# Kernel tuning notes

Hardware: AMD Instinct MI355X
Metric: run time of the kernel (lower is better)

The kernel has to match this reference:

```python
import jax, jax.numpy as jnp
import numpy as np

N_NODES = 20000   # N
N_EDGES = 320000  # E (avg degree 16)
T_STEPS = 16      # T
IN_FEATS = 1      # F
HG = 64           # hidden_g
HT = 128          # hidden_t
LN_EPS = 1e-5


def _layer_norm(x, g, b):
    mu = jnp.mean(x, axis=-1, keepdims=True)
    var = jnp.mean((x - mu) ** 2, axis=-1, keepdims=True)
    return (x - mu) * jax.lax.rsqrt(var + LN_EPS) * g + b


def setup_inputs() -> dict:
    key = jax.random.key(0)
    k = jax.random.split(key, 16)
    r = lambda i, shape, s: jax.random.normal(k[i], shape, jnp.float32) * s
    return dict(
        x_seq=jax.random.normal(k[0], (1, T_STEPS, N_NODES, IN_FEATS), jnp.float32),
        edge_index=jax.random.randint(k[1], (2, N_EDGES), 0, N_NODES, dtype=jnp.int32),
        # SAGEConv layer 0: lin_l (aggregated neighbors, has bias) + lin_r (root)
        W_l0=r(2, (IN_FEATS, HG), 0.5), W_r0=r(3, (IN_FEATS, HG), 0.5), b0=jnp.zeros((HG,), jnp.float32),
        ln0_g=jnp.ones((HG,), jnp.float32), ln0_b=jnp.zeros((HG,), jnp.float32),
        # SAGEConv layer 1
        W_l1=r(4, (HG, HG), 0.1), W_r1=r(5, (HG, HG), 0.1), b1=jnp.zeros((HG,), jnp.float32),
        ln1_g=jnp.ones((HG,), jnp.float32), ln1_b=jnp.zeros((HG,), jnp.float32),
        # GRU (torch layout: gates r,z,n stacked along first dim)
        gru_Wih=r(6, (3 * HT, HG), 0.05), gru_Whh=r(7, (3 * HT, HT), 0.05),
        gru_bih=jnp.zeros((3 * HT,), jnp.float32), gru_bhh=jnp.zeros((3 * HT,), jnp.float32),
        # head
        head_W=r(8, (HT, 1), 0.05), head_b=jnp.zeros((1,), jnp.float32),
    )


def reference(x_seq, edge_index, W_l0, W_r0, b0, ln0_g, ln0_b,
              W_l1, W_r1, b1, ln1_g, ln1_b,
              gru_Wih, gru_Whh, gru_bih, gru_bhh, head_W, head_b):
    src, dst = edge_index[0], edge_index[1]
    # in-degree for mean aggregation (clamped to 1, like PyG mean aggr on isolated nodes)
    deg = jnp.clip(jax.ops.segment_sum(jnp.ones((N_EDGES,), jnp.float32), dst,
                                       num_segments=N_NODES), 1.0)[:, None]

    def sage(x, Wl, Wr, b):
        # mean over incoming neighbors, then lin_l(aggr) + lin_r(root)
        agg = jax.ops.segment_sum(x[src], dst, num_segments=N_NODES) / deg
        return agg @ Wl + x @ Wr + b

    def stack(xt):  # xt: (N, F) -> (N, HG); dropout is identity in eval mode
        h = jax.nn.relu(_layer_norm(sage(xt, W_l0, W_r0, b0), ln0_g, ln0_b))
        h = jax.nn.relu(_layer_norm(sage(h, W_l1, W_r1, b1), ln1_g, ln1_b))
        return h

    X = x_seq[0]  # (T, N, F), B == 1
    # scan over timesteps (matches the per-t Python loop, bounds peak memory)
    _, H = jax.lax.scan(lambda c, xt: (c, stack(xt)), None, X)  # H: (T, N, HG)

    def gru_step(h, xt):  # torch GRU cell; batch = N nodes
        gi = xt @ gru_Wih.T + gru_bih
        gh = h @ gru_Whh.T + gru_bhh
        ir, iz, inn = jnp.split(gi, 3, axis=-1)
        hr, hz, hn = jnp.split(gh, 3, axis=-1)
        r = jax.nn.sigmoid(ir + hr)
        z = jax.nn.sigmoid(iz + hz)
        n = jnp.tanh(inn + r * hn)
        return (1.0 - z) * n + z * h, None

    h0 = jnp.zeros((N_NODES, HT), x_seq.dtype)
    hT, _ = jax.lax.scan(gru_step, h0, H)
    y = (hT @ head_W + head_b)[:, 0]  # (N,)
    return y
```

## Files before the change

### kernel.cpp

```cpp
#include <hip/hip_runtime.h>
#include <math.h>

#define NN 20000
#define NE 320000
#define TS 16
#define HG 64
#define HTT 128
#define NG 384
#define LN_EPS 1e-5f

typedef __attribute__((ext_vector_type(8))) _Float16 f16x8;
typedef __attribute__((ext_vector_type(4))) _Float16 f16x4;
typedef __attribute__((ext_vector_type(2))) _Float16 f16x2;
typedef __attribute__((ext_vector_type(4))) float f32x4;

__device__ __forceinline__ float wave_sum64(float v) {
  #pragma unroll
  for (int off = 32; off > 0; off >>= 1) v += __shfl_xor(v, off, 64);
  return v;
}
__device__ __forceinline__ float quad_sum16(float v) {
  #pragma unroll
  for (int off = 1; off < 16; off <<= 1) v += __shfl_xor(v, off, 64);
  return v;
}
__device__ __forceinline__ float fast_sigmoid(float x) {
  return __builtin_amdgcn_rcpf(1.f + __expf(-x));
}
__device__ __forceinline__ float fast_tanh(float x) {
  float e = __expf(-2.f * fabsf(x));
  float th = (1.f - e) * __builtin_amdgcn_rcpf(1.f + e);
  return copysignf(th, x);
}


__global__ __launch_bounds__(256) void k_setup(
    const float* __restrict__ x_seq, float* __restrict__ xT,
    const float* __restrict__ Wih, _Float16* __restrict__ WihF,
    const float* __restrict__ Whh, _Float16* __restrict__ WhhF,
    const float* __restrict__ Wl1, const float* __restrict__ Wr1,
    _Float16* __restrict__ Wchi, _Float16* __restrict__ Wclo,
    const float* __restrict__ Wl0, const float* __restrict__ Wr0,
    const float* __restrict__ b0, const float* __restrict__ g0,
    const float* __restrict__ be0, float* __restrict__ P,
    int* __restrict__ cnt) {
  int gid = blockIdx.x * 256 + threadIdx.x;
  int stride = gridDim.x * 256;
  for (int i = gid; i < NN * TS; i += stride) {
    int t = i / NN, n = i - t * NN;
    xT[n * 16 + t] = x_seq[i];
  }
  for (int i = gid; i < NG * HG; i += stride) WihF[i] = (_Float16)Wih[i];
  for (int i = gid; i < NG * HTT; i += stride) WhhF[i] = (_Float16)Whh[i];
  for (int i = gid; i < HG * 128; i += stride) {
    int n = i >> 7, k = i & 127;
    float x = (k < HG) ? Wl1[k * HG + n] : Wr1[(k - HG) * HG + n];
    _Float16 h = (_Float16)x;
    Wchi[i] = h;
    Wclo[i] = (_Float16)(x - (float)h);
  }
  for (int i = gid; i < NN; i += stride) cnt[i] = 0;
  if (blockIdx.x == 0 && threadIdx.x < 64) {
    int f = threadIdx.x;
    float u = Wl0[f], v = Wr0[f], c = b0[f], g = g0[f];
    float um = wave_sum64(u) * (1.f / 64.f);
    float vm = wave_sum64(v) * (1.f / 64.f);
    float cm = wave_sum64(c) * (1.f / 64.f);
    float uc = u - um, vc = v - vm, cc = c - cm;
    float muu = wave_sum64(uc * uc) * (1.f / 64.f);
    float mvv = wave_sum64(vc * vc) * (1.f / 64.f);
    float mcc = wave_sum64(cc * cc) * (1.f / 64.f);
    float muv = wave_sum64(uc * vc) * (1.f / 64.f);
    float muc = wave_sum64(uc * cc) * (1.f / 64.f);
    float mvc = wave_sum64(vc * cc) * (1.f / 64.f);
    P[f] = uc * g; P[64 + f] = vc * g; P[128 + f] = cc * g; P[192 + f] = be0[f];
    if (f == 0) {
      P[256] = muu; P[257] = mvv; P[258] = mcc;
      P[259] = muv; P[260] = muc; P[261] = mvc;
    }
  }
}

__global__ void k_hist(const int* __restrict__ dst, int* cnt) {
  int e = blockIdx.x * blockDim.x + threadIdx.x;
  if (e < NE) atomicAdd(&cnt[dst[e]], 1);
}

__global__ void k_scan(int* cnt, int* row_ptr, float* deg_inv) {
  __shared__ int s[1024];
  const int PER = 20;
  int tid = threadIdx.x;
  int base = tid * PER;
  int vloc[PER], dloc[PER];
  int sum = 0;
  #pragma unroll
  for (int j = 0; j < PER; j++) {
    int n = base + j;
    int d = (n < NN) ? cnt[n] : 0;
    vloc[j] = sum;
    dloc[j] = d;
    sum += d;
  }
  s[tid] = sum;
  __syncthreads();
  for (int off = 1; off < 1024; off <<= 1) {
    int t = (tid >= off) ? s[tid - off] : 0;
    __syncthreads();
    s[tid] += t;
    __syncthreads();
  }
  int excl = s[tid] - sum;
  #pragma unroll
  for (int j = 0; j < PER; j++) {
    int n = base + j;
    if (n < NN) {
      int rp = excl + vloc[j];
      row_ptr[n] = rp;
      cnt[n] = rp;
      int d = dloc[j];
      deg_inv[n] = 1.0f / (float)((d > 1) ? d : 1);
    }
  }
  if (tid == 1023) row_ptr[NN] = s[1023];
}

__global__ void k_fill(const int* __restrict__ src, const int* __restrict__ dst,
                       int* cursor, int* col) {
  int e = blockIdx.x * blockDim.x + threadIdx.x;
  if (e < NE) {
    int p = atomicAdd(&cursor[dst[e]], 1);
    col[p] = src[e];
  }
}

__global__ __launch_bounds__(256) void k_h0_fused(
    const float* __restrict__ xT,
    const int* __restrict__ row_ptr, const int* __restrict__ col,
    const float* __restrict__ deg_inv,
    const float* __restrict__ P,
    _Float16* __restrict__ h0r,
    _Float16* __restrict__ code2) {
  int lane = threadIdx.x & 63;
  int n = blockIdx.x * 4 + (threadIdx.x >> 6);
  int grp = lane >> 4, tl = lane & 15;
  int beg = row_ptr[n];
  int deg = row_ptr[n + 1] - beg;
  float s0 = 0.f, s1 = 0.f;
  int iters = (deg + 7) >> 3;
  for (int it = 0; it < iters; it++) {
    int e0 = it * 8 + grp, e1 = it * 8 + 4 + grp;
    bool v0 = e0 < deg, v1 = e1 < deg;
    int i0 = v0 ? e0 : 0, i1 = v1 ? e1 : 0;
    int c0 = col[beg + i0];
    int c1 = col[beg + i1];
    float x0 = xT[c0 * 16 + tl];
    float x1 = xT[c1 * 16 + tl];
    s0 += v0 ? x0 : 0.f;
    s1 += v1 ? x1 : 0.f;
  }
  float s = s0 + s1;
  s += __shfl_xor(s, 16, 64);
  s += __shfl_xor(s, 32, 64);
  float aggv = s * deg_inv[n];
  float xv = xT[n * 16 + tl];
  float muu = P[256], mvv = P[257], mcc = P[258];
  float muv = P[259], muc = P[260], mvc = P[261];
  if (lane < 16) {
    float a = aggv, x = xv;
    float var = a * a * muu + x * x * mvv + mcc
              + 2.f * (a * x * muv + a * muc + x * mvc);
    float rstd = rsqrtf(var + LN_EPS);
    _Float16 Ah = (_Float16)(a * rstd);
    _Float16 Xh = (_Float16)(x * rstd);
    _Float16 Ch = (_Float16)rstd;
    f16x8 cw = {Ah, Ah, Xh, Xh, Ch, Ch, (_Float16)0.f, (_Float16)0.f};
    *(f16x8*)&code2[(size_t)n * 128 + (lane & 7) * 16 + (lane >> 3) * 8] = cw;
  }
  #pragma unroll
  for (int half = 0; half < 2; half++) {
    int c = lane + half * 64;
    int t = c >> 3, f8 = (c & 7) * 8;
    float a = __shfl(aggv, t, 64);
    float x = __shfl(xv, t, 64);
    float var = a * a * muu + x * x * mvv + mcc
              + 2.f * (a * x * muv + a * muc + x * mvc);
    float rstd = rsqrtf(var + LN_EPS);
    f16x8 o;
    #pragma unroll
    for (int j = 0; j < 8; j++) {
      int f = f8 + j;
      float d = a * P[f] + x * P[64 + f] + P[128 + f];
      o[j] = (_Float16)fmaxf(d * rstd + P[192 + f], 0.f);
    }
    *(f16x8*)&h0r[(size_t)n * 1024 + c * 8] = o;
  }
}

__global__ __launch_bounds__(256) void k_gather(
    const int* __restrict__ row_ptr, const int* __restrict__ col,
    const _Float16* __restrict__ code2,
    const float* __restrict__ P,
    _Float16* __restrict__ agg) {
  int lane = threadIdx.x & 63;
  int n = blockIdx.x * 4 + (threadIdx.x >> 6);
  const f16x2 h2z = {(_Float16)0.f, (_Float16)0.f};
  const f16x2 h2o = {(_Float16)1.f, (_Float16)1.f};
  int f1 = (lane & 7) * 8;
  int tmod = lane >> 3;
  f16x2 Pu2[4], Pv2[4], Pc2[4], Pb2[4];
  #pragma unroll
  for (int j = 0; j < 4; j++) {
    Pu2[j] = (f16x2){(_Float16)P[f1 + 2*j],       (_Float16)P[f1 + 2*j + 1]};
    Pv2[j] = (f16x2){(_Float16)P[64 + f1 + 2*j],  (_Float16)P[64 + f1 + 2*j + 1]};
    Pc2[j] = (f16x2){(_Float16)P[128 + f1 + 2*j], (_Float16)P[128 + f1 + 2*j + 1]};
    Pb2[j] = (f16x2){(_Float16)P[192 + f1 + 2*j], (_Float16)P[192 + f1 + 2*j + 1]};
  }
  int beg = row_ptr[n];
  int deg = row_ptr[n + 1] - beg;
  int cvAll = (lane < deg) ? col[beg + lane] : 0;

  f16x2 aE1[4], aO1[4], aE2[4], aO2[4];
  #pragma unroll
  for (int j = 0; j < 4; j++) { aE1[j] = h2z; aO1[j] = h2z; aE2[j] = h2z; aO2[j] = h2z; }

#define ACC_SET(c, mk, FULL, ACC)                                          \
  { f16x2 _A = __builtin_shufflevector(c, c, 0, 1);                        \
    f16x2 _X = __builtin_shufflevector(c, c, 2, 3);                        \
    f16x2 _C = __builtin_shufflevector(c, c, 4, 5);                        \
    _Pragma("unroll")                                                      \
    for (int j = 0; j < 4; j++) {                                          \
      f16x2 d = __builtin_elementwise_fma(_A, Pu2[j],                      \
                 __builtin_elementwise_fma(_X, Pv2[j],                     \
                  __builtin_elementwise_fma(_C, Pc2[j], Pb2[j])));         \
      d = __builtin_elementwise_max(d, h2z);                               \
      ACC[j] = (FULL) ? (ACC[j] + d)                                       \
                      : __builtin_elementwise_fma(d, mk, ACC[j]);          \
    } }

  int nb4 = (deg + 3) >> 2;
  if (nb4 > 16) nb4 = 16;
  for (int b = 0; b < nb4; b++) {
    int eb = b << 2;
    f16x8 cA[4], cB[4];
    #pragma unroll
    for (int e = 0; e < 4; e++) {
      int c = __builtin_amdgcn_readlane(cvAll, eb + e);
      const _Float16* cp = code2 + (size_t)c * 128 + tmod * 16;
      cA[e] = *(const f16x8*)cp;
      cB[e] = *(const f16x8*)(cp + 8);
    }
    if (eb + 4 <= deg) {
      #pragma unroll
      for (int e = 0; e < 4; e++) {
        if (e & 1) { ACC_SET(cA[e], h2o, true, aO1) ACC_SET(cB[e], h2o, true, aO2) }
        else       { ACC_SET(cA[e], h2o, true, aE1) ACC_SET(cB[e], h2o, true, aE2) }
      }
    } else {
      #pragma unroll
      for (int e = 0; e < 4; e++) {
        f16x2 mk = ((eb + e) < deg) ? h2o : h2z;
        if (e & 1) { ACC_SET(cA[e], mk, false, aO1) ACC_SET(cB[e], mk, false, aO2) }
        else       { ACC_SET(cA[e], mk, false, aE1) ACC_SET(cB[e], mk, false, aE2) }
      }
    }
  }
  for (int e = 64; e < deg; e++) {
    int c = col[beg + e];
    const _Float16* cp = code2 + (size_t)c * 128 + tmod * 16;
    f16x8 ca = *(const f16x8*)cp;
    f16x8 cb = *(const f16x8*)(cp + 8);
    ACC_SET(ca, h2o, true, aE1) ACC_SET(cb, h2o, true, aE2)
  }
#undef ACC_SET

  float dif = 1.0f / (float)((deg > 1) ? deg : 1);
  _Float16 dih = (_Float16)dif;
  f16x2 di2 = {dih, dih};
  union { f16x8 v; f16x2 h[4]; } u0, u1;
  #pragma unroll
  for (int j = 0; j < 4; j++) {
    u0.h[j] = (aE1[j] + aO1[j]) * di2;
    u1.h[j] = (aE2[j] + aO2[j]) * di2;
  }
  *(f16x8*)&agg[(size_t)n * 1024 + lane * 8] = u0.v;
  *(f16x8*)&agg[(size_t)n * 1024 + 512 + lane * 8] = u1.v;
}

__global__ __launch_bounds__(256) void k_gemm(
    const _Float16* __restrict__ h0r,
    const _Float16* __restrict__ agg,
    const _Float16* __restrict__ Wchi, const _Float16* __restrict__ Wclo,
    const float* __restrict__ b1, const float* __restrict__ g1, const float* __restrict__ be1,
    _Float16* __restrict__ Ht_all) {
  int tid = threadIdx.x;
  int lane = tid & 63, wave = tid >> 6;
  int col16 = lane & 15, quad = lane >> 4;
  int m0 = blockIdx.x * 16;

  float bias[4], gg[4], bb[4];
  #pragma unroll
  for (int nt = 0; nt < 4; nt++) {
    int nf = nt * 16 + col16;
    bias[nt] = b1[nf]; gg[nt] = g1[nf]; bb[nt] = be1[nf];
  }
  size_t rowbase = (size_t)(m0 + col16) * 1024;

  for (int ts = 0; ts < 4; ts++) {
    int t = wave * 4 + ts;
    f32x4 acc[4];
    #pragma unroll
    for (int nt = 0; nt < 4; nt++) acc[nt] = (f32x4){0.f, 0.f, 0.f, 0.f};

    f16x8 aa[2], ar[2];
    #pragma unroll
    for (int kk = 0; kk < 2; kk++) {
      aa[kk] = *(const f16x8*)&agg[rowbase + t * 64 + kk * 32 + quad * 8];
      ar[kk] = *(const f16x8*)&h0r[rowbase + t * 64 + kk * 32 + quad * 8];
    }
    #pragma unroll
    for (int kk = 0; kk < 2; kk++) {
      #pragma unroll
      for (int nt = 0; nt < 4; nt++) {
        int nf = nt * 16 + col16;
        f16x8 bh = *(const f16x8*)&Wchi[nf * 128 + kk * 32 + quad * 8];
        f16x8 bl = *(const f16x8*)&Wclo[nf * 128 + kk * 32 + quad * 8];
        acc[nt] = __builtin_amdgcn_mfma_f32_16x16x32_f16(aa[kk], bh, acc[nt], 0, 0, 0);
        acc[nt] = __builtin_amdgcn_mfma_f32_16x16x32_f16(aa[kk], bl, acc[nt], 0, 0, 0);
      }
    }
    #pragma unroll
    for (int kk = 0; kk < 2; kk++) {
      #pragma unroll
      for (int nt = 0; nt < 4; nt++) {
        int nf = nt * 16 + col16;
        f16x8 bh = *(const f16x8*)&Wchi[nf * 128 + 64 + kk * 32 + quad * 8];
        f16x8 bl = *(const f16x8*)&Wclo[nf * 128 + 64 + kk * 32 + quad * 8];
        acc[nt] = __builtin_amdgcn_mfma_f32_16x16x32_f16(ar[kk], bh, acc[nt], 0, 0, 0);
        acc[nt] = __builtin_amdgcn_mfma_f32_16x16x32_f16(ar[kk], bl, acc[nt], 0, 0, 0);
      }
    }

    #pragma unroll
    for (int r = 0; r < 4; r++) {
      float v[4];
      #pragma unroll
      for (int nt = 0; nt < 4; nt++) v[nt] = acc[nt][r] + bias[nt];
      float s = (v[0] + v[1]) + (v[2] + v[3]);
      float mu = quad_sum16(s) * (1.f / 64.f);
      float sq = 0.f;
      #pragma unroll
      for (int nt = 0; nt < 4; nt++) { v[nt] -= mu; sq += v[nt] * v[nt]; }
      float var = quad_sum16(sq) * (1.f / 64.f);
      float rstd = rsqrtf(var + LN_EPS);
      int m = m0 + quad * 4 + r;
      size_t base = ((size_t)t * NN + m) * HG;
      #pragma unroll
      for (int nt = 0; nt < 4; nt++) {
        float o = fmaxf(v[nt] * rstd * gg[nt] + bb[nt], 0.f);
        Ht_all[base + nt * 16 + col16] = (_Float16)o;
      }
    }
  }
}

__global__ __launch_bounds__(256, 2) void k_gru_all(
    const _Float16* __restrict__ Ht_all,
    const _Float16* __restrict__ WihF,
    const _Float16* __restrict__ WhhF,
    const float* __restrict__ bih, const float* __restrict__ bhh,
    const float* __restrict__ headW, const float* __restrict__ headb,
    float* __restrict__ out) {
  __shared__ _Float16 WihL[NG * 64];
  __shared__ _Float16 hL[2][32 * 128];
  __shared__ float yL[4][32];

  int tid = threadIdx.x;
  int lane = tid & 63, wave = tid >> 6;
  int col16 = lane & 15, quad = lane >> 4;
  int m0 = blockIdx.x * 32;
  int gb = 2 * wave;

  for (int i = tid; i < NG * 8; i += 256) {
    int g = i >> 3, k8 = i & 7;
    *(f16x8*)&WihL[g * 64 + ((k8 + g) & 7) * 8] = *(const f16x8*)&WihF[g * 64 + k8 * 8];
  }
  for (int i = tid; i < 2 * 32 * 128; i += 256) hL[0][i] = (_Float16)0.f;

  int gts[6];
  #pragma unroll
  for (int t6 = 0; t6 < 6; t6++)
    gts[t6] = (t6 < 2) ? (gb + t6) : (t6 < 4) ? (8 + gb + t6 - 2) : (16 + gb + t6 - 4);

  f16x8 wgh[4][6];
  #pragma unroll
  for (int kk = 0; kk < 4; kk++)
    #pragma unroll
    for (int t6 = 0; t6 < 6; t6++)
      wgh[kk][t6] = *(const f16x8*)&WhhF[(size_t)(gts[t6] * 16 + col16) * HTT + kk * 32 + quad * 8];

  float bR[2], bZ[2], bNi[2], bNh[2], hw[2];
  int waddr[2][4][2];
  #pragma unroll
  for (int js = 0; js < 2; js++) {
    int j = (gb + js) * 16 + col16;
    bR[js]  = bih[j] + bhh[j];
    bZ[js]  = bih[HTT + j] + bhh[HTT + j];
    bNi[js] = bih[2 * HTT + j];
    bNh[js] = bhh[2 * HTT + j];
    hw[js]  = headW[j];
    #pragma unroll
    for (int mt = 0; mt < 2; mt++)
      #pragma unroll
      for (int r = 0; r < 4; r++) {
        int row = mt * 16 + quad * 4 + r;
        waddr[mt][r][js] = row * 128 + (((j >> 3) + row) & 15) * 8 + (j & 7);
      }
  }
  float hreg[2][4][2];
  #pragma unroll
  for (int mt = 0; mt < 2; mt++)
    #pragma unroll
    for (int r = 0; r < 4; r++) { hreg[mt][r][0] = 0.f; hreg[mt][r][1] = 0.f; }

  size_t aoff[2][2];
  #pragma unroll
  for (int kk = 0; kk < 2; kk++)
    #pragma unroll
    for (int mt = 0; mt < 2; mt++)
      aoff[kk][mt] = (size_t)(m0 + mt * 16 + col16) * HG + kk * 32 + quad * 8;

  __syncthreads();

  for (int t = 0; t < TS; t++) {
    const _Float16* hcur = hL[t & 1];
    _Float16* hnxt = hL[(t + 1) & 1];

    f32x4 acc[8][2];
    #pragma unroll
    for (int a = 0; a < 8; a++) {
      acc[a][0] = (f32x4){0.f, 0.f, 0.f, 0.f};
      acc[a][1] = (f32x4){0.f, 0.f, 0.f, 0.f};
    }

    const _Float16* AH = Ht_all + (size_t)t * NN * HG;
    f16x8 gah[2][2];
    #pragma unroll
    for (int kk = 0; kk < 2; kk++)
      #pragma unroll
      for (int mt = 0; mt < 2; mt++)
        gah[kk][mt] = *(const f16x8*)&AH[aoff[kk][mt]];

    #pragma unroll
    for (int kk = 0; kk < 4; kk++) {
      f16x8 ah[2];
      #pragma unroll
      for (int mt = 0; mt < 2; mt++) {
        int row = mt * 16 + col16;
        int k8 = kk * 4 + quad;
        ah[mt] = *(const f16x8*)&hcur[row * 128 + ((k8 + row) & 15) * 8];
      }
      #pragma unroll
      for (int t6 = 0; t6 < 6; t6++) {
        int ai = (t6 < 4) ? t6 : t6 + 2;
        #pragma unroll
        for (int mt = 0; mt < 2; mt++)
          acc[ai][mt] = __builtin_amdgcn_mfma_f32_16x16x32_f16(ah[mt], wgh[kk][t6], acc[ai][mt], 0, 0, 0);
      }
    }
    #pragma unroll
    for (int kk = 0; kk < 2; kk++) {
      #pragma unroll
      for (int t6 = 0; t6 < 6; t6++) {
        int g = gts[t6] * 16 + col16;
        int k8 = kk * 4 + quad;
        f16x8 b = *(const f16x8*)&WihL[g * 64 + ((k8 + g) & 7) * 8];
        #pragma unroll
        for (int mt = 0; mt < 2; mt++)
          acc[t6][mt] = __builtin_amdgcn_mfma_f32_16x16x32_f16(gah[kk][mt], b, acc[t6][mt], 0, 0, 0);
      }
    }

    #pragma unroll
    for (int mt = 0; mt < 2; mt++) {
      #pragma unroll
      for (int r = 0; r < 4; r++) {
        #pragma unroll
        for (int js = 0; js < 2; js++) {
          float R  = acc[0 + js][mt][r] + bR[js];
          float Z  = acc[2 + js][mt][r] + bZ[js];
          float Ni = acc[4 + js][mt][r] + bNi[js];
          float Nh = acc[6 + js][mt][r] + bNh[js];
          float rg = fast_sigmoid(R);
          float zg = fast_sigmoid(Z);
          float nn = fast_tanh(Ni + rg * Nh);
          float hn = nn + zg * (hreg[mt][r][js] - nn);
          hreg[mt][r][js] = hn;
          hnxt[waddr[mt][r][js]] = (_Float16)hn;
        }
      }
    }
    __syncthreads();
  }

  #pragma unroll
  for (int mt = 0; mt < 2; mt++) {
    #pragma unroll
    for (int r = 0; r < 4; r++) {
      float py = hreg[mt][r][0] * hw[0] + hreg[mt][r][1] * hw[1];
      py = quad_sum16(py);
      if (col16 == 0) yL[wave][mt * 16 + quad * 4 + r] = py;
    }
  }
  __syncthreads();
  if (tid < 32)
    out[m0 + tid] = yL[0][tid] + yL[1][tid] + yL[2][tid] + yL[3][tid] + headb[0];
}

extern "C" void kernel_launch(void* const* d_in, const int* in_sizes, int n_in,
                              void* d_out, int out_size, void* d_ws, size_t ws_size,
                              hipStream_t stream) {
  const float* x_seq = (const float*)d_in[0];
  const int*   edge  = (const int*)d_in[1];
  const float* Wl0   = (const float*)d_in[2];
  const float* Wr0   = (const float*)d_in[3];
  const float* b0    = (const float*)d_in[4];
  const float* g0    = (const float*)d_in[5];
  const float* be0   = (const float*)d_in[6];
  const float* Wl1   = (const float*)d_in[7];
  const float* Wr1   = (const float*)d_in[8];
  const float* b1    = (const float*)d_in[9];
  const float* g1    = (const float*)d_in[10];
  const float* be1   = (const float*)d_in[11];
  const float* Wih   = (const float*)d_in[12];
  const float* Whh   = (const float*)d_in[13];
  const float* bih   = (const float*)d_in[14];
  const float* bhh   = (const float*)d_in[15];
  const float* headW = (const float*)d_in[16];
  const float* headb = (const float*)d_in[17];
  float* out = (float*)d_out;

  const int* srcp = edge;
  const int* dstp = edge + NE;

  char* ws = (char*)d_ws;
  size_t off = 0;
  auto alloc = [&](size_t bytes) -> void* {
    void* p = ws + off;
    off += (bytes + 255) & ~(size_t)255;
    return p;
  };
  int*   cnt     = (int*)alloc(NN * 4);
  int*   row_ptr = (int*)alloc((NN + 1) * 4);
  int*   col     = (int*)alloc(NE * 4);
  float* deg_inv = (float*)alloc(NN * 4);
  float* xT      = (float*)alloc((size_t)NN * TS * 4);
  float* P       = (float*)alloc(512 * 4);
  _Float16* h0r  = (_Float16*)alloc((size_t)NN * 1024 * 2);
  _Float16* code2= (_Float16*)alloc((size_t)NN * 128 * 2);
  _Float16* agg  = (_Float16*)alloc((size_t)NN * 1024 * 2);
  _Float16* Ht_all = (_Float16*)alloc((size_t)TS * NN * HG * 2);
  _Float16* WihF = (_Float16*)alloc((size_t)NG * HG * 2);
  _Float16* WhhF = (_Float16*)alloc((size_t)NG * HTT * 2);
  _Float16* Wchi = (_Float16*)alloc((size_t)HG * 128 * 2);
  _Float16* Wclo = (_Float16*)alloc((size_t)HG * 128 * 2);
  (void)ws_size; (void)in_sizes; (void)n_in; (void)out_size;

  k_setup<<<1250, 256, 0, stream>>>(x_seq, xT, Wih, WihF, Whh, WhhF,
                                    Wl1, Wr1, Wchi, Wclo,
                                    Wl0, Wr0, b0, g0, be0, P, cnt);
  k_hist<<<(NE + 255) / 256, 256, 0, stream>>>(dstp, cnt);
  k_scan<<<1, 1024, 0, stream>>>(cnt, row_ptr, deg_inv);
  k_fill<<<(NE + 255) / 256, 256, 0, stream>>>(srcp, dstp, cnt, col);
  k_h0_fused<<<NN / 4, 256, 0, stream>>>(xT, row_ptr, col, deg_inv, P, h0r, code2);
  k_gather<<<NN / 4, 256, 0, stream>>>(row_ptr, col, code2, P, agg);
  k_gemm<<<NN / 16, 256, 0, stream>>>(h0r, agg, Wchi, Wclo, b1, g1, be1, Ht_all);
  k_gru_all<<<NN / 32, 256, 0, stream>>>(Ht_all, WihF, WhhF, bih, bhh,
                                         headW, headb, out);
}
```

Measured before the change: 361.9 us.

## Restructure GRU kernel to 64-row tiles with 8 waves and single h buffer

The GRU kernel now uses 512-thread blocks over 64 node rows, with each of 8 waves owning one 16-column slice of the hidden state instead of two. The recurrent-weight fragments held in registers per wave are halved. The ping-pong h buffer is replaced by a single shared buffer guarded by an extra barrier per timestep. The goal is to cut register pressure, amortize the shared Wih copy over more rows, and raise occupancy, at the cost of one more __syncthreads per step and a clamped tail block.

```diff
diff --git a/kernel.cpp b/kernel.cpp
--- a/kernel.cpp
+++ b/kernel.cpp
@@ -363,7 +363,7 @@
   }
 }
 
-__global__ __launch_bounds__(256, 2) void k_gru_all(
+__global__ __launch_bounds__(512, 4) void k_gru_all(
     const _Float16* __restrict__ Ht_all,
     const _Float16* __restrict__ WihF,
     const _Float16* __restrict__ WhhF,
@@ -371,149 +371,133 @@
     const float* __restrict__ headW, const float* __restrict__ headb,
     float* __restrict__ out) {
   __shared__ _Float16 WihL[NG * 64];
-  __shared__ _Float16 hL[2][32 * 128];
-  __shared__ float yL[4][32];
+  __shared__ _Float16 hL[64 * 128];
 
   int tid = threadIdx.x;
   int lane = tid & 63, wave = tid >> 6;
   int col16 = lane & 15, quad = lane >> 4;
-  int m0 = blockIdx.x * 32;
-  int gb = 2 * wave;
-
-  for (int i = tid; i < NG * 8; i += 256) {
+  int m0 = blockIdx.x * 64;
+
+  for (int i = tid; i < NG * 8; i += 512) {
     int g = i >> 3, k8 = i & 7;
     *(f16x8*)&WihL[g * 64 + ((k8 + g) & 7) * 8] = *(const f16x8*)&WihF[g * 64 + k8 * 8];
   }
-  for (int i = tid; i < 2 * 32 * 128; i += 256) hL[0][i] = (_Float16)0.f;
-
-  int gts[6];
-  #pragma unroll
-  for (int t6 = 0; t6 < 6; t6++)
-    gts[t6] = (t6 < 2) ? (gb + t6) : (t6 < 4) ? (8 + gb + t6 - 2) : (16 + gb + t6 - 4);
-
-  f16x8 wgh[4][6];
+  for (int i = tid; i < 64 * 128; i += 512) hL[i] = (_Float16)0.f;
+
+  int gts3[3] = {wave, 8 + wave, 16 + wave};
+
+  f16x8 wgh[4][3];
   #pragma unroll
   for (int kk = 0; kk < 4; kk++)
     #pragma unroll
-    for (int t6 = 0; t6 < 6; t6++)
-      wgh[kk][t6] = *(const f16x8*)&WhhF[(size_t)(gts[t6] * 16 + col16) * HTT + kk * 32 + quad * 8];
-
-  float bR[2], bZ[2], bNi[2], bNh[2], hw[2];
-  int waddr[2][4][2];
-  #pragma unroll
-  for (int js = 0; js < 2; js++) {
-    int j = (gb + js) * 16 + col16;
-    bR[js]  = bih[j] + bhh[j];
-    bZ[js]  = bih[HTT + j] + bhh[HTT + j];
-    bNi[js] = bih[2 * HTT + j];
-    bNh[js] = bhh[2 * HTT + j];
-    hw[js]  = headW[j];
-    #pragma unroll
-    for (int mt = 0; mt < 2; mt++)
-      #pragma unroll
-      for (int r = 0; r < 4; r++) {
-        int row = mt * 16 + quad * 4 + r;
-        waddr[mt][r][js] = row * 128 + (((j >> 3) + row) & 15) * 8 + (j & 7);
-      }
-  }
-  float hreg[2][4][2];
-  #pragma unroll
-  for (int mt = 0; mt < 2; mt++)
-    #pragma unroll
-    for (int r = 0; r < 4; r++) { hreg[mt][r][0] = 0.f; hreg[mt][r][1] = 0.f; }
-
-  size_t aoff[2][2];
-  #pragma unroll
-  for (int kk = 0; kk < 2; kk++)
-    #pragma unroll
-    for (int mt = 0; mt < 2; mt++)
-      aoff[kk][mt] = (size_t)(m0 + mt * 16 + col16) * HG + kk * 32 + quad * 8;
+    for (int g3 = 0; g3 < 3; g3++)
+      wgh[kk][g3] = *(const f16x8*)&WhhF[(size_t)(gts3[g3] * 16 + col16) * HTT + kk * 32 + quad * 8];
+
+  int j = wave * 16 + col16;
+  float bR  = bih[j] + bhh[j];
+  float bZ  = bih[HTT + j] + bhh[HTT + j];
+  float bNi = bih[2 * HTT + j];
+  float bNh = bhh[2 * HTT + j];
+  float hw  = headW[j];
+  int jsw = j >> 3, jlo = j & 7;
+
+  float hreg[4][4];
+  #pragma unroll
+  for (int mt = 0; mt < 4; mt++)
+    #pragma unroll
+    for (int r = 0; r < 4; r++) hreg[mt][r] = 0.f;
 
   __syncthreads();
 
   for (int t = 0; t < TS; t++) {
-    const _Float16* hcur = hL[t & 1];
-    _Float16* hnxt = hL[(t + 1) & 1];
-
-    f32x4 acc[8][2];
-    #pragma unroll
-    for (int a = 0; a < 8; a++) {
-      acc[a][0] = (f32x4){0.f, 0.f, 0.f, 0.f};
-      acc[a][1] = (f32x4){0.f, 0.f, 0.f, 0.f};
-    }
-
-    const _Float16* AH = Ht_all + (size_t)t * NN * HG;
-    f16x8 gah[2][2];
-    #pragma unroll
-    for (int kk = 0; kk < 2; kk++)
-      #pragma unroll
-      for (int mt = 0; mt < 2; mt++)
-        gah[kk][mt] = *(const f16x8*)&AH[aoff[kk][mt]];
+    f32x4 acc[4][4];
+    #pragma unroll
+    for (int a = 0; a < 4; a++)
+      #pragma unroll
+      for (int mt = 0; mt < 4; mt++)
+        acc[a][mt] = (f32x4){0.f, 0.f, 0.f, 0.f};
 
     #pragma unroll
     for (int kk = 0; kk < 4; kk++) {
-      f16x8 ah[2];
-      #pragma unroll
-      for (int mt = 0; mt < 2; mt++) {
+      f16x8 ah[4];
+      #pragma unroll
+      for (int mt = 0; mt < 4; mt++) {
         int row = mt * 16 + col16;
         int k8 = kk * 4 + quad;
-        ah[mt] = *(const f16x8*)&hcur[row * 128 + ((k8 + row) & 15) * 8];
-      }
-      #pragma unroll
-      for (int t6 = 0; t6 < 6; t6++) {
-        int ai = (t6 < 4) ? t6 : t6 + 2;
+        ah[mt] = *(const f16x8*)&hL[row * 128 + ((k8 + row) & 15) * 8];
+      }
+      #pragma unroll
+      for (int g3 = 0; g3 < 3; g3++) {
+        int ai = (g3 == 2) ? 3 : g3;
         #pragma unroll
-        for (int mt = 0; mt < 2; mt++)
-          acc[ai][mt] = __builtin_amdgcn_mfma_f32_16x16x32_f16(ah[mt], wgh[kk][t6], acc[ai][mt], 0, 0, 0);
-      }
-    }
-    #pragma unroll
-    for (int kk = 0; kk < 2; kk++) {
-      #pragma unroll
-      for (int t6 = 0; t6 < 6; t6++) {
-        int g = gts[t6] * 16 + col16;
-        int k8 = kk * 4 + quad;
-        f16x8 b = *(const f16x8*)&WihL[g * 64 + ((k8 + g) & 7) * 8];
+        for (int mt = 0; mt < 4; mt++)
+          acc[ai][mt] = __builtin_amdgcn_mfma_f32_16x16x32_f16(ah[mt], wgh[kk][g3], acc[ai][mt], 0, 0, 0);
+      }
+    }
+
+    {
+      const _Float16* AH = Ht_all + (size_t)t * NN * HG;
+      #pragma unroll
+      for (int kk = 0; kk < 2; kk++) {
+        f16x8 ga[4];
         #pragma unroll
-        for (int mt = 0; mt < 2; mt++)
-          acc[t6][mt] = __builtin_amdgcn_mfma_f32_16x16x32_f16(gah[kk][mt], b, acc[t6][mt], 0, 0, 0);
-      }
-    }
-
-    #pragma unroll
-    for (int mt = 0; mt < 2; mt++) {
+        for (int mt = 0; mt < 4; mt++) {
+          int rowg = m0 + mt * 16 + col16;
+          if (rowg >= NN) rowg = NN - 1;
+          ga[mt] = *(const f16x8*)&AH[(size_t)rowg * HG + kk * 32 + quad * 8];
+        }
+        #pragma unroll
+        for (int g3 = 0; g3 < 3; g3++) {
+          int g = gts3[g3] * 16 + col16;
+          int k8 = kk * 4 + quad;
+          f16x8 b = *(const f16x8*)&WihL[g * 64 + ((k8 + g) & 7) * 8];
+          int ai = (g3 == 2) ? 2 : g3;
+          #pragma unroll
+          for (int mt = 0; mt < 4; mt++)
+            acc[ai][mt] = __builtin_amdgcn_mfma_f32_16x16x32_f16(ga[mt], b, acc[ai][mt], 0, 0, 0);
+        }
+      }
+    }
+
+    __syncthreads();
+
+    #pragma unroll
+    for (int mt = 0; mt < 4; mt++) {
       #pragma unroll
       for (int r = 0; r < 4; r++) {
-        #pragma unroll
-        for (int js = 0; js < 2; js++) {
-          float R  = acc[0 + js][mt][r] + bR[js];
-          float Z  = acc[2 + js][mt][r] + bZ[js];
-          float Ni = acc[4 + js][mt][r] + bNi[js];
-          float Nh = acc[6 + js][mt][r] + bNh[js];
-          float rg = fast_sigmoid(R);
-          float zg = fast_sigmoid(Z);
-          float nn = fast_tanh(Ni + rg * Nh);
-          float hn = nn + zg * (hreg[mt][r][js] - nn);
-          hreg[mt][r][js] = hn;
-          hnxt[waddr[mt][r][js]] = (_Float16)hn;
-        }
+        float R  = acc[0][mt][r] + bR;
+        float Z  = acc[1][mt][r] + bZ;
+        float Ni = acc[2][mt][r] + bNi;
+        float Nh = acc[3][mt][r] + bNh;
+        float rg = fast_sigmoid(R);
+        float zg = fast_sigmoid(Z);
+        float nn = fast_tanh(Ni + rg * Nh);
+        float hn = nn + zg * (hreg[mt][r] - nn);
+        hreg[mt][r] = hn;
+        int row = mt * 16 + quad * 4 + r;
+        hL[row * 128 + ((jsw + row) & 15) * 8 + jlo] = (_Float16)hn;
       }
     }
     __syncthreads();
   }
 
-  #pragma unroll
-  for (int mt = 0; mt < 2; mt++) {
+  float* yL = (float*)hL;
+  #pragma unroll
+  for (int mt = 0; mt < 4; mt++) {
     #pragma unroll
     for (int r = 0; r < 4; r++) {
-      float py = hreg[mt][r][0] * hw[0] + hreg[mt][r][1] * hw[1];
+      float py = hreg[mt][r] * hw;
       py = quad_sum16(py);
-      if (col16 == 0) yL[wave][mt * 16 + quad * 4 + r] = py;
+      if (col16 == 0) yL[wave * 64 + mt * 16 + quad * 4 + r] = py;
     }
   }
   __syncthreads();
-  if (tid < 32)
-    out[m0 + tid] = yL[0][tid] + yL[1][tid] + yL[2][tid] + yL[3][tid] + headb[0];
+  if (tid < 64 && m0 + tid < NN) {
+    float s = 0.f;
+    #pragma unroll
+    for (int w = 0; w < 8; w++) s += yL[w * 64 + tid];
+    out[m0 + tid] = s + headb[0];
+  }
 }
 
 extern "C" void kernel_launch(void* const* d_in, const int* in_sizes, int n_in,
@@ -574,6 +558,6 @@
   k_h0_fused<<<NN / 4, 256, 0, stream>>>(xT, row_ptr, col, deg_inv, P, h0r, code2);
   k_gather<<<NN / 4, 256, 0, stream>>>(row_ptr, col, code2, P, agg);
   k_gemm<<<NN / 16, 256, 0, stream>>>(h0r, agg, Wchi, Wclo, b1, g1, be1, Ht_all);
-  k_gru_all<<<NN / 32, 256, 0, stream>>>(Ht_all, WihF, WhhF, bih, bhh,
-                                         headW, headb, out);
-}
+  k_gru_all<<<(NN + 63) / 64, 512, 0, stream>>>(Ht_all, WihF, WhhF, bih, bhh,
+                                                headW, headb, out);
+}
```

After: 501.3 us. 1.39x slower.

## Widen GRU blocks to 64 nodes and single-buffer hidden state in LDS

Applied to the files above, without the earlier changes.

The GRU kernel now launches 512-thread blocks, each covering 64 nodes as two 32-row halves. This amortises the shared-memory load of the input weight matrix over twice as many nodes. The hidden-state buffer is now single-buffered, with an extra barrier per step before the write-back, which cuts LDS per node but adds a sync each timestep. Tail rows are clamped because 20000 is not a multiple of 64, and the launch-bounds occupancy hint is removed.

```diff
diff --git a/kernel.cpp b/kernel.cpp
--- a/kernel.cpp
+++ b/kernel.cpp
@@ -363,7 +363,7 @@
   }
 }
 
-__global__ __launch_bounds__(256, 2) void k_gru_all(
+__global__ __launch_bounds__(512) void k_gru_all(
     const _Float16* __restrict__ Ht_all,
     const _Float16* __restrict__ WihF,
     const _Float16* __restrict__ WhhF,
@@ -371,20 +371,22 @@
     const float* __restrict__ headW, const float* __restrict__ headb,
     float* __restrict__ out) {
   __shared__ _Float16 WihL[NG * 64];
-  __shared__ _Float16 hL[2][32 * 128];
-  __shared__ float yL[4][32];
+  __shared__ _Float16 hL[64 * 128];
+  __shared__ float yL[8][32];
 
   int tid = threadIdx.x;
   int lane = tid & 63, wave = tid >> 6;
+  int half = wave >> 2, w4 = wave & 3;
   int col16 = lane & 15, quad = lane >> 4;
-  int m0 = blockIdx.x * 32;
-  int gb = 2 * wave;
-
-  for (int i = tid; i < NG * 8; i += 256) {
+  int m0 = blockIdx.x * 64 + half * 32;
+  int rbase = half * 32;
+  int gb = 2 * w4;
+
+  for (int i = tid; i < NG * 8; i += 512) {
     int g = i >> 3, k8 = i & 7;
     *(f16x8*)&WihL[g * 64 + ((k8 + g) & 7) * 8] = *(const f16x8*)&WihF[g * 64 + k8 * 8];
   }
-  for (int i = tid; i < 2 * 32 * 128; i += 256) hL[0][i] = (_Float16)0.f;
+  for (int i = tid; i < 64 * 128; i += 512) hL[i] = (_Float16)0.f;
 
   int gts[6];
   #pragma unroll
@@ -412,7 +414,7 @@
     for (int mt = 0; mt < 2; mt++)
       #pragma unroll
       for (int r = 0; r < 4; r++) {
-        int row = mt * 16 + quad * 4 + r;
+        int row = rbase + mt * 16 + quad * 4 + r;
         waddr[mt][r][js] = row * 128 + (((j >> 3) + row) & 15) * 8 + (j & 7);
       }
   }
@@ -426,15 +428,15 @@
   #pragma unroll
   for (int kk = 0; kk < 2; kk++)
     #pragma unroll
-    for (int mt = 0; mt < 2; mt++)
-      aoff[kk][mt] = (size_t)(m0 + mt * 16 + col16) * HG + kk * 32 + quad * 8;
+    for (int mt = 0; mt < 2; mt++) {
+      int rowg = m0 + mt * 16 + col16;
+      if (rowg >= NN) rowg = NN - 1;
+      aoff[kk][mt] = (size_t)rowg * HG + kk * 32 + quad * 8;
+    }
 
   __syncthreads();
 
   for (int t = 0; t < TS; t++) {
-    const _Float16* hcur = hL[t & 1];
-    _Float16* hnxt = hL[(t + 1) & 1];
-
     f32x4 acc[8][2];
     #pragma unroll
     for (int a = 0; a < 8; a++) {
@@ -455,9 +457,9 @@
       f16x8 ah[2];
       #pragma unroll
       for (int mt = 0; mt < 2; mt++) {
-        int row = mt * 16 + col16;
+        int row = rbase + mt * 16 + col16;
         int k8 = kk * 4 + quad;
-        ah[mt] = *(const f16x8*)&hcur[row * 128 + ((k8 + row) & 15) * 8];
+        ah[mt] = *(const f16x8*)&hL[row * 128 + ((k8 + row) & 15) * 8];
       }
       #pragma unroll
       for (int t6 = 0; t6 < 6; t6++) {
@@ -493,12 +495,20 @@
           float rg = fast_sigmoid(R);
           float zg = fast_sigmoid(Z);
           float nn = fast_tanh(Ni + rg * Nh);
-          float hn = nn + zg * (hreg[mt][r][js] - nn);
-          hreg[mt][r][js] = hn;
-          hnxt[waddr[mt][r][js]] = (_Float16)hn;
+          hreg[mt][r][js] = nn + zg * (hreg[mt][r][js] - nn);
         }
       }
     }
+
+    __syncthreads();
+
+    #pragma unroll
+    for (int mt = 0; mt < 2; mt++)
+      #pragma unroll
+      for (int r = 0; r < 4; r++)
+        #pragma unroll
+        for (int js = 0; js < 2; js++)
+          hL[waddr[mt][r][js]] = (_Float16)hreg[mt][r][js];
     __syncthreads();
   }
 
@@ -512,8 +522,14 @@
     }
   }
   __syncthreads();
-  if (tid < 32)
-    out[m0 + tid] = yL[0][tid] + yL[1][tid] + yL[2][tid] + yL[3][tid] + headb[0];
+  if (tid < 64) {
+    int n = blockIdx.x * 64 + tid;
+    if (n < NN) {
+      int ho = (tid >> 5) * 4;
+      int idx = tid & 31;
+      out[n] = yL[ho + 0][idx] + yL[ho + 1][idx] + yL[ho + 2][idx] + yL[ho + 3][idx] + headb[0];
+    }
+  }
 }
 
 extern "C" void kernel_launch(void* const* d_in, const int* in_sizes, int n_in,
@@ -574,6 +590,6 @@
   k_h0_fused<<<NN / 4, 256, 0, stream>>>(xT, row_ptr, col, deg_inv, P, h0r, code2);
   k_gather<<<NN / 4, 256, 0, stream>>>(row_ptr, col, code2, P, agg);
   k_gemm<<<NN / 16, 256, 0, stream>>>(h0r, agg, Wchi, Wclo, b1, g1, be1, Ht_all);
-  k_gru_all<<<NN / 32, 256, 0, stream>>>(Ht_all, WihF, WhhF, bih, bhh,
-                                         headW, headb, out);
-}
+  k_gru_all<<<(NN + 63) / 64, 512, 0, stream>>>(Ht_all, WihF, WhhF, bih, bhh,
+                                                headW, headb, out);
+}
```

After: 386.7 us. +6.9%, slower.
